# Optimization experiments

Measured on AMD Instinct MI355X. Metric: run time of the kernel, lower is better.

Reference implementation:

```python
import jax, jax.numpy as jnp
import numpy as np

N = 50000
E = 1600000
H, C = 4, 32
NEG_SLOPE = 0.2
EPS = 1e-16


def _l2norm_row(a):
    # F.normalize(a, p=2, dim=1) for a of shape [1, F]
    return a / jnp.maximum(jnp.linalg.norm(a, axis=1, keepdims=True), 1e-12)


def setup_inputs() -> dict:
    key = jax.random.key(0)
    ks = jax.random.split(key, 7)
    x = jax.random.normal(ks[0], (N, 256), dtype=jnp.float32)
    edge_index = jax.random.randint(ks[1], (2, E), 0, N, dtype=jnp.int32)
    v_mapping = jax.random.normal(ks[2], (64, 256), dtype=jnp.float32) * 0.1
    W_src = jax.random.normal(ks[3], (256, H * C), dtype=jnp.float32) * 0.06
    att_src = jax.random.normal(ks[4], (1, 64), dtype=jnp.float32)
    att_dst = jax.random.normal(ks[5], (1, 64), dtype=jnp.float32)
    bias = jnp.zeros((H * C,), dtype=jnp.float32)
    return {"x": x, "edge_index": edge_index, "v_mapping": v_mapping,
            "W_src": W_src, "att_src": att_src, "att_dst": att_dst, "bias": bias}


def reference(x, edge_index, v_mapping, W_src, att_src, att_dst, bias):
    # node projection: [N, H, C]
    x_proj = (x @ W_src).reshape(-1, H, C)
    # attention-locator scores: scalar per node
    score = x @ v_mapping.T                      # [N, F]
    a_src = (score * _l2norm_row(att_src)).sum(-1)  # [N]
    a_dst = (score * _l2norm_row(att_dst)).sum(-1)  # [N]

    src, dst = edge_index[0], edge_index[1]
    alpha = a_src[src] + a_dst[dst]              # [E]
    alpha = jax.nn.leaky_relu(alpha, NEG_SLOPE)
    # segment softmax over destination nodes
    m = jax.ops.segment_max(alpha, dst, num_segments=N)
    alpha = jnp.exp(alpha - jax.lax.stop_gradient(m)[dst])
    denom = jax.ops.segment_sum(alpha, dst, num_segments=N)
    alpha = alpha / (denom[dst] + EPS)           # [E]

    msg = x_proj[src] * alpha[:, None, None]     # [E, H, C]
    agg = jax.ops.segment_sum(msg, dst, num_segments=N)  # [N, H, C]

    out = x_proj + agg                           # residual as in forward
    out = out.reshape(-1, H * C) + bias          # concat heads + bias
    return out
```

## Files before the change

### kernel.cpp

```cpp
#include <hip/hip_runtime.h>

#define N_NODES 50000
#define E_EDGES 1600000
#define HC 128
#define NEG_SLOPE 0.2f
#define SM_EPS 1e-16f
#define NBKT 782
#define BKT_STRIDE 2600
#define EPB1 3072
#define NB1 521

typedef __attribute__((ext_vector_type(8))) short short8v;
typedef __attribute__((ext_vector_type(4))) float f32x4;

__device__ inline unsigned bf16pack(float a, float b) {
  unsigned ua = __float_as_uint(a), ub = __float_as_uint(b);
  ua = (ua + 0x7fffu + ((ua >> 16) & 1u)) >> 16;
  ub = (ub + 0x7fffu + ((ub >> 16) & 1u)) >> 16;
  return ua | (ub << 16);
}

__global__ __launch_bounds__(256) void k0_init(
    const float* __restrict__ v_mapping,
    const float* __restrict__ att_src,
    const float* __restrict__ att_dst,
    const float* __restrict__ W,
    unsigned short* __restrict__ wT,
    int* __restrict__ gcursor) {
  const int tid = threadIdx.x, bid = blockIdx.x;
  if (bid < 4) {
    const int i = bid * 256 + tid;
    if (i < NBKT) gcursor[i] = i * BKT_STRIDE;
  }

  __shared__ float wv[2][256];
  {
    const int j = tid;
    float ns = 0.f, nd = 0.f;
    for (int f = 0; f < 64; ++f) {
      float a = att_src[f]; ns = fmaf(a, a, ns);
      float b = att_dst[f]; nd = fmaf(b, b, nd);
    }
    ns = fmaxf(sqrtf(ns), 1e-12f);
    nd = fmaxf(sqrtf(nd), 1e-12f);
    float s = 0.f, d = 0.f;
    for (int f = 0; f < 64; ++f) {
      float v = v_mapping[f * 256 + j];
      s = fmaf(v, att_src[f], s);
      d = fmaf(v, att_dst[f], d);
    }
    wv[0][j] = s / ns;
    wv[1][j] = d / nd;
  }
  __syncthreads();

#pragma unroll
  for (int r = 0; r < 8; ++r) {
    const int n = bid * 8 + r;
    const int k = tid;
    float v;
    if (n < 128) v = W[k * 128 + n];
    else if (n == 128) v = wv[0][k];
    else if (n == 129) v = wv[1][k];
    else v = 0.f;
    unsigned u = __float_as_uint(v);
    u = (u + 0x7fffu + ((u >> 16) & 1u)) >> 16;
    wT[n * 256 + k] = (unsigned short)u;
  }
}

__global__ __launch_bounds__(256) void k1_node(
    const float* __restrict__ x,
    const unsigned short* __restrict__ wT,
    unsigned* __restrict__ xpb,
    float* __restrict__ a_src, float* __restrict__ a_dst) {
  __shared__ unsigned short xs[64 * 264];
  const int tid = threadIdx.x;
  const int w = tid >> 6, lane = tid & 63;
  const int rowbase = blockIdx.x * 64;

  const float4* x4 = (const float4*)x;
#pragma unroll
  for (int c = 0; c < 16; ++c) {
    const int idx = c * 256 + tid;
    const int row = idx >> 6, c4 = idx & 63;
    float4 v = make_float4(0.f, 0.f, 0.f, 0.f);
    if (rowbase + row < N_NODES) v = x4[(size_t)(rowbase + row) * 64 + c4];
    uint2 p;
    p.x = bf16pack(v.x, v.y);
    p.y = bf16pack(v.z, v.w);
    *(uint2*)&xs[row * 264 + c4 * 4] = p;
  }
  __syncthreads();

  f32x4 acc[9];
#pragma unroll
  for (int t = 0; t < 9; ++t) acc[t] = (f32x4){0.f, 0.f, 0.f, 0.f};

  const int m = lane & 15, kq = lane >> 4;
  const unsigned short* arow = &xs[(w * 16 + m) * 264 + kq * 8];
#pragma unroll
  for (int ks = 0; ks < 8; ++ks) {
    const short8v af = *(const short8v*)(arow + ks * 32);
#pragma unroll
    for (int ct = 0; ct < 9; ++ct) {
      const short8v bf = *(const short8v*)(wT + (ct * 16 + m) * 256 + ks * 32 + kq * 8);
      acc[ct] = __builtin_amdgcn_mfma_f32_16x16x32_bf16(af, bf, acc[ct], 0, 0, 0);
    }
  }

  if (m < 2) {
    float* ap = m ? a_dst : a_src;
#pragma unroll
    for (int i = 0; i < 4; ++i) {
      const int rg = rowbase + w * 16 + kq * 4 + i;
      if (rg < N_NODES) ap[rg] = acc[8][i];
    }
  }

  float* cs = (float*)&xs[w * 16 * 264];
#pragma unroll
  for (int ct = 0; ct < 8; ++ct)
#pragma unroll
    for (int i = 0; i < 4; ++i)
      cs[(kq * 4 + i) * 132 + ct * 16 + m] = acc[ct][i];
  __syncthreads();

  const int prow = lane & 15, q = lane >> 4;
  const int grow = rowbase + w * 16 + prow;
  unsigned uu[16];
#pragma unroll
  for (int u = 0; u < 16; ++u) {
    const float2 f2 = *(const float2*)&cs[prow * 132 + q * 32 + u * 2];
    uu[u] = bf16pack(f2.x, f2.y);
  }
  if (grow < N_NODES) {
    uint4* d4 = (uint4*)&xpb[(size_t)grow * 64 + q * 16];
    d4[0] = make_uint4(uu[0], uu[1], uu[2], uu[3]);
    d4[1] = make_uint4(uu[4], uu[5], uu[6], uu[7]);
    d4[2] = make_uint4(uu[8], uu[9], uu[10], uu[11]);
    d4[3] = make_uint4(uu[12], uu[13], uu[14], uu[15]);
  }
}

__global__ __launch_bounds__(1024) void kc1_coarse(
    const int* __restrict__ ei,
    const float* __restrict__ a_src, const float* __restrict__ a_dst,
    int* __restrict__ gcursor, int2* __restrict__ coarse) {
  __shared__ int chist[NBKT];
  __shared__ int gbase[NBKT];
  __shared__ int ccur[NBKT];
  const int tid = threadIdx.x;
  const int ebase = blockIdx.x * EPB1;
  for (int b = tid; b < NBKT; b += 1024) { chist[b] = 0; ccur[b] = 0; }
  __syncthreads();

#pragma unroll
  for (int i = 0; i < 3; ++i) {
    const int e = ebase + i * 1024 + tid;
    if (e < E_EDGES) atomicAdd(&chist[ei[E_EDGES + e] >> 6], 1);
  }
  __syncthreads();

  for (int b = tid; b < NBKT; b += 1024) {
    const int c = chist[b];
    if (c > 0) gbase[b] = atomicAdd(&gcursor[b], c);
  }
  __syncthreads();

#pragma unroll
  for (int i = 0; i < 3; ++i) {
    const int e = ebase + i * 1024 + tid;
    if (e < E_EDGES) {
      const int s = ei[e];
      const int d = ei[E_EDGES + e];
      const int b = d >> 6;
      float a = a_src[s] + a_dst[d];
      a = a > 0.f ? a : NEG_SLOPE * a;
      const float ev = __expf(a);
      const int pos = gbase[b] + atomicAdd(&ccur[b], 1);
      if (pos < (b + 1) * BKT_STRIDE)
        coarse[pos] = make_int2(s | ((d & 63) << 16), __float_as_int(ev));
    }
  }
}

__global__ __launch_bounds__(1024) void kc2_reduce(
    const int* __restrict__ gcursor, const int2* __restrict__ coarse,
    const unsigned* __restrict__ xpb,
    const float* __restrict__ bias,
    float* __restrict__ out) {
  __shared__ unsigned sorted[BKT_STRIDE];
  __shared__ int hist[64], cur[64];
  __shared__ int base[65];
  const int b = blockIdx.x;
  const int tid = threadIdx.x;
  const int cstart = b * BKT_STRIDE;
  const int cnt = min(gcursor[b] - cstart, BKT_STRIDE);

  if (tid < 64) { hist[tid] = 0; cur[tid] = 0; }
  __syncthreads();

  for (int j = tid; j < cnt; j += 1024)
    atomicAdd(&hist[(coarse[cstart + j].x >> 16) & 63], 1);
  __syncthreads();

  if (tid < 64) {
    const int h = hist[tid];
    int inc = h;
#pragma unroll
    for (int off = 1; off < 64; off <<= 1) {
      int t = __shfl_up(inc, off);
      if (tid >= off) inc += t;
    }
    base[tid] = inc - h;
    if (tid == 63) base[64] = inc;
  }
  __syncthreads();

  for (int j = tid; j < cnt; j += 1024) {
    const int2 e2 = coarse[cstart + j];
    const int dloc = (e2.x >> 16) & 63;
    unsigned uev = (unsigned)e2.y;
    uev = (uev + 0x7fffu + ((uev >> 16) & 1u)) >> 16;
    const int p = base[dloc] + atomicAdd(&cur[dloc], 1);
    sorted[p] = (unsigned)(e2.x & 0xffff) | (uev << 16);
  }
  __syncthreads();

  const int g = tid >> 4, gl = tid & 15;
  const int dst = (b << 6) | g;
  if (dst >= N_NODES) return;

  const uint4* xp4 = (const uint4*)xpb;
  const float4* br = (const float4*)bias;
  const float4 b0 = br[2 * gl], b1 = br[2 * gl + 1];

  const int s0 = base[g];
  const int cntd = base[g + 1] - s0;

  float acc[8];
#pragma unroll
  for (int i = 0; i < 8; ++i) acc[i] = 0.f;
  float den = 0.f;

  int j = 0;
  for (; j + 4 <= cntd; j += 4) {
    unsigned u[4];
    float ev[4];
    uint4 v[4];
#pragma unroll
    for (int t = 0; t < 4; ++t) {
      u[t] = sorted[s0 + j + t];
      ev[t] = __uint_as_float(u[t] & 0xffff0000u);
      v[t] = xp4[(size_t)(u[t] & 0xffffu) * 16 + gl];
    }
#pragma unroll
    for (int t = 0; t < 4; ++t) {
      den += ev[t];
      acc[0] = fmaf(ev[t], __uint_as_float(v[t].x << 16), acc[0]);
      acc[1] = fmaf(ev[t], __uint_as_float(v[t].x & 0xffff0000u), acc[1]);
      acc[2] = fmaf(ev[t], __uint_as_float(v[t].y << 16), acc[2]);
      acc[3] = fmaf(ev[t], __uint_as_float(v[t].y & 0xffff0000u), acc[3]);
      acc[4] = fmaf(ev[t], __uint_as_float(v[t].z << 16), acc[4]);
      acc[5] = fmaf(ev[t], __uint_as_float(v[t].z & 0xffff0000u), acc[5]);
      acc[6] = fmaf(ev[t], __uint_as_float(v[t].w << 16), acc[6]);
      acc[7] = fmaf(ev[t], __uint_as_float(v[t].w & 0xffff0000u), acc[7]);
    }
  }
  for (; j < cntd; ++j) {
    const unsigned u = sorted[s0 + j];
    const float ev = __uint_as_float(u & 0xffff0000u);
    const uint4 v = xp4[(size_t)(u & 0xffffu) * 16 + gl];
    den += ev;
    acc[0] = fmaf(ev, __uint_as_float(v.x << 16), acc[0]);
    acc[1] = fmaf(ev, __uint_as_float(v.x & 0xffff0000u), acc[1]);
    acc[2] = fmaf(ev, __uint_as_float(v.y << 16), acc[2]);
    acc[3] = fmaf(ev, __uint_as_float(v.y & 0xffff0000u), acc[3]);
    acc[4] = fmaf(ev, __uint_as_float(v.z << 16), acc[4]);
    acc[5] = fmaf(ev, __uint_as_float(v.z & 0xffff0000u), acc[5]);
    acc[6] = fmaf(ev, __uint_as_float(v.w << 16), acc[6]);
    acc[7] = fmaf(ev, __uint_as_float(v.w & 0xffff0000u), acc[7]);
  }

  const float inv = 1.f / (den + SM_EPS);
  const uint4 ur = xp4[(size_t)dst * 16 + gl];
  float4 o0, o1;
  o0.x = __uint_as_float(ur.x << 16)         + b0.x + acc[0] * inv;
  o0.y = __uint_as_float(ur.x & 0xffff0000u) + b0.y + acc[1] * inv;
  o0.z = __uint_as_float(ur.y << 16)         + b0.z + acc[2] * inv;
  o0.w = __uint_as_float(ur.y & 0xffff0000u) + b0.w + acc[3] * inv;
  o1.x = __uint_as_float(ur.z << 16)         + b1.x + acc[4] * inv;
  o1.y = __uint_as_float(ur.z & 0xffff0000u) + b1.y + acc[5] * inv;
  o1.z = __uint_as_float(ur.w << 16)         + b1.z + acc[6] * inv;
  o1.w = __uint_as_float(ur.w & 0xffff0000u) + b1.w + acc[7] * inv;
  float4* orow = (float4*)(out + (size_t)dst * HC);
  orow[2 * gl] = o0;
  orow[2 * gl + 1] = o1;
}

extern "C" void kernel_launch(void* const* d_in, const int* in_sizes, int n_in,
                              void* d_out, int out_size, void* d_ws, size_t ws_size,
                              hipStream_t stream) {
  const float* x         = (const float*)d_in[0];
  const int*   ei        = (const int*)d_in[1];
  const float* v_mapping = (const float*)d_in[2];
  const float* W_src     = (const float*)d_in[3];
  const float* att_src   = (const float*)d_in[4];
  const float* att_dst   = (const float*)d_in[5];
  const float* bias      = (const float*)d_in[6];
  float* out = (float*)d_out;

  char* ws = (char*)d_ws;
  unsigned*       xpb     = (unsigned*)ws;        ws += (size_t)N_NODES * 64 * 4;
  float*          a_src   = (float*)ws;           ws += (size_t)N_NODES * 4;
  float*          a_dst   = (float*)ws;           ws += (size_t)N_NODES * 4;
  unsigned short* wT      = (unsigned short*)ws;  ws += 144 * 256 * 2;
  int*            gcursor = (int*)ws;             ws += ((NBKT + 127) / 128) * 128 * 4;
  int2*           coarse  = (int2*)ws;            ws += (size_t)NBKT * BKT_STRIDE * 8;

  k0_init<<<18, 256, 0, stream>>>(v_mapping, att_src, att_dst, W_src, wT, gcursor);
  k1_node<<<(N_NODES + 63) / 64, 256, 0, stream>>>(x, wT, xpb, a_src, a_dst);
  kc1_coarse<<<NB1, 1024, 0, stream>>>(ei, a_src, a_dst, gcursor, coarse);
  kc2_reduce<<<NBKT, 1024, 0, stream>>>(gcursor, coarse, xpb, bias, out);
}
```

Baseline: 151.8 us.

## Fuse edge bucketing into node GEMM kernel and defer exp to reduce

```diff
diff --git a/kernel.cpp b/kernel.cpp
--- a/kernel.cpp
+++ b/kernel.cpp
@@ -7,8 +7,7 @@
 #define SM_EPS 1e-16f
 #define NBKT 782
 #define BKT_STRIDE 2600
-#define EPB1 3072
-#define NB1 521
+#define EPBH 2048
 
 typedef __attribute__((ext_vector_type(8))) short short8v;
 typedef __attribute__((ext_vector_type(4))) float f32x4;
@@ -69,15 +68,56 @@
   }
 }
 
-__global__ __launch_bounds__(256) void k1_node(
+__global__ __launch_bounds__(256) void k1_fused(
     const float* __restrict__ x,
     const unsigned short* __restrict__ wT,
     unsigned* __restrict__ xpb,
-    float* __restrict__ a_src, float* __restrict__ a_dst) {
-  __shared__ unsigned short xs[64 * 264];
+    float* __restrict__ a_src, float* __restrict__ a_dst,
+    const int* __restrict__ ei,
+    int* __restrict__ gcursor, unsigned* __restrict__ coarse) {
+  __shared__ char smem[64 * 264 * 2];
+  const int bid = blockIdx.x;
   const int tid = threadIdx.x;
+
+  if (bid & 1) {
+    int* chist = (int*)smem;
+    int* gbase = (int*)(smem + 3200);
+    int* ccur  = (int*)(smem + 6400);
+    const int ebase = (bid >> 1) * EPBH;
+    for (int b = tid; b < NBKT; b += 256) { chist[b] = 0; ccur[b] = 0; }
+    __syncthreads();
+
+#pragma unroll
+    for (int i = 0; i < 8; ++i) {
+      const int e = ebase + i * 256 + tid;
+      if (e < E_EDGES) atomicAdd(&chist[ei[E_EDGES + e] >> 6], 1);
+    }
+    __syncthreads();
+
+    for (int b = tid; b < NBKT; b += 256) {
+      const int c = chist[b];
+      if (c > 0) gbase[b] = atomicAdd(&gcursor[b], c);
+    }
+    __syncthreads();
+
+#pragma unroll
+    for (int i = 0; i < 8; ++i) {
+      const int e = ebase + i * 256 + tid;
+      if (e < E_EDGES) {
+        const int s = ei[e];
+        const int d = ei[E_EDGES + e];
+        const int b = d >> 6;
+        const int pos = gbase[b] + atomicAdd(&ccur[b], 1);
+        if (pos < (b + 1) * BKT_STRIDE)
+          coarse[pos] = (unsigned)s | ((unsigned)(d & 63) << 16);
+      }
+    }
+    return;
+  }
+
+  unsigned short* xs = (unsigned short*)smem;
   const int w = tid >> 6, lane = tid & 63;
-  const int rowbase = blockIdx.x * 64;
+  const int rowbase = (bid >> 1) * 64;
 
   const float4* x4 = (const float4*)x;
 #pragma unroll
@@ -118,7 +158,7 @@
     }
   }
 
-  float* cs = (float*)&xs[w * 16 * 264];
+  float* cs = (float*)(smem + (size_t)w * 16 * 264 * 2);
 #pragma unroll
   for (int ct = 0; ct < 8; ++ct)
 #pragma unroll
@@ -143,66 +183,30 @@
   }
 }
 
-__global__ __launch_bounds__(1024) void kc1_coarse(
-    const int* __restrict__ ei,
+__global__ __launch_bounds__(512) void kc2_reduce(
+    const int* __restrict__ gcursor, const unsigned* __restrict__ coarse,
     const float* __restrict__ a_src, const float* __restrict__ a_dst,
-    int* __restrict__ gcursor, int2* __restrict__ coarse) {
-  __shared__ int chist[NBKT];
-  __shared__ int gbase[NBKT];
-  __shared__ int ccur[NBKT];
-  const int tid = threadIdx.x;
-  const int ebase = blockIdx.x * EPB1;
-  for (int b = tid; b < NBKT; b += 1024) { chist[b] = 0; ccur[b] = 0; }
-  __syncthreads();
-
-#pragma unroll
-  for (int i = 0; i < 3; ++i) {
-    const int e = ebase + i * 1024 + tid;
-    if (e < E_EDGES) atomicAdd(&chist[ei[E_EDGES + e] >> 6], 1);
-  }
-  __syncthreads();
-
-  for (int b = tid; b < NBKT; b += 1024) {
-    const int c = chist[b];
-    if (c > 0) gbase[b] = atomicAdd(&gcursor[b], c);
-  }
-  __syncthreads();
-
-#pragma unroll
-  for (int i = 0; i < 3; ++i) {
-    const int e = ebase + i * 1024 + tid;
-    if (e < E_EDGES) {
-      const int s = ei[e];
-      const int d = ei[E_EDGES + e];
-      const int b = d >> 6;
-      float a = a_src[s] + a_dst[d];
-      a = a > 0.f ? a : NEG_SLOPE * a;
-      const float ev = __expf(a);
-      const int pos = gbase[b] + atomicAdd(&ccur[b], 1);
-      if (pos < (b + 1) * BKT_STRIDE)
-        coarse[pos] = make_int2(s | ((d & 63) << 16), __float_as_int(ev));
-    }
-  }
-}
-
-__global__ __launch_bounds__(1024) void kc2_reduce(
-    const int* __restrict__ gcursor, const int2* __restrict__ coarse,
     const unsigned* __restrict__ xpb,
     const float* __restrict__ bias,
     float* __restrict__ out) {
   __shared__ unsigned sorted[BKT_STRIDE];
   __shared__ int hist[64], cur[64];
   __shared__ int base[65];
+  __shared__ float adl[64];
   const int b = blockIdx.x;
   const int tid = threadIdx.x;
   const int cstart = b * BKT_STRIDE;
   const int cnt = min(gcursor[b] - cstart, BKT_STRIDE);
 
-  if (tid < 64) { hist[tid] = 0; cur[tid] = 0; }
-  __syncthreads();
-
-  for (int j = tid; j < cnt; j += 1024)
-    atomicAdd(&hist[(coarse[cstart + j].x >> 16) & 63], 1);
+  if (tid < 64) {
+    hist[tid] = 0; cur[tid] = 0;
+    const int dg = (b << 6) | tid;
+    adl[tid] = (dg < N_NODES) ? a_dst[dg] : 0.f;
+  }
+  __syncthreads();
+
+  for (int j = tid; j < cnt; j += 512)
+    atomicAdd(&hist[(coarse[cstart + j] >> 16) & 63], 1);
   __syncthreads();
 
   if (tid < 64) {
@@ -218,85 +222,89 @@
   }
   __syncthreads();
 
-  for (int j = tid; j < cnt; j += 1024) {
-    const int2 e2 = coarse[cstart + j];
-    const int dloc = (e2.x >> 16) & 63;
-    unsigned uev = (unsigned)e2.y;
+  for (int j = tid; j < cnt; j += 512) {
+    const unsigned e2 = coarse[cstart + j];
+    const int src = e2 & 0xffffu;
+    const int dloc = (e2 >> 16) & 63;
+    float a = a_src[src] + adl[dloc];
+    a = a > 0.f ? a : NEG_SLOPE * a;
+    unsigned uev = __float_as_uint(__expf(a));
     uev = (uev + 0x7fffu + ((uev >> 16) & 1u)) >> 16;
     const int p = base[dloc] + atomicAdd(&cur[dloc], 1);
-    sorted[p] = (unsigned)(e2.x & 0xffff) | (uev << 16);
+    sorted[p] = (unsigned)src | (uev << 16);
   }
   __syncthreads();
 
   const int g = tid >> 4, gl = tid & 15;
-  const int dst = (b << 6) | g;
-  if (dst >= N_NODES) return;
-
   const uint4* xp4 = (const uint4*)xpb;
   const float4* br = (const float4*)bias;
   const float4 b0 = br[2 * gl], b1 = br[2 * gl + 1];
 
-  const int s0 = base[g];
-  const int cntd = base[g + 1] - s0;
-
-  float acc[8];
-#pragma unroll
-  for (int i = 0; i < 8; ++i) acc[i] = 0.f;
-  float den = 0.f;
-
-  int j = 0;
-  for (; j + 4 <= cntd; j += 4) {
-    unsigned u[4];
-    float ev[4];
-    uint4 v[4];
-#pragma unroll
-    for (int t = 0; t < 4; ++t) {
-      u[t] = sorted[s0 + j + t];
-      ev[t] = __uint_as_float(u[t] & 0xffff0000u);
-      v[t] = xp4[(size_t)(u[t] & 0xffffu) * 16 + gl];
-    }
-#pragma unroll
-    for (int t = 0; t < 4; ++t) {
-      den += ev[t];
-      acc[0] = fmaf(ev[t], __uint_as_float(v[t].x << 16), acc[0]);
-      acc[1] = fmaf(ev[t], __uint_as_float(v[t].x & 0xffff0000u), acc[1]);
-      acc[2] = fmaf(ev[t], __uint_as_float(v[t].y << 16), acc[2]);
-      acc[3] = fmaf(ev[t], __uint_as_float(v[t].y & 0xffff0000u), acc[3]);
-      acc[4] = fmaf(ev[t], __uint_as_float(v[t].z << 16), acc[4]);
-      acc[5] = fmaf(ev[t], __uint_as_float(v[t].z & 0xffff0000u), acc[5]);
-      acc[6] = fmaf(ev[t], __uint_as_float(v[t].w << 16), acc[6]);
-      acc[7] = fmaf(ev[t], __uint_as_float(v[t].w & 0xffff0000u), acc[7]);
-    }
-  }
-  for (; j < cntd; ++j) {
-    const unsigned u = sorted[s0 + j];
-    const float ev = __uint_as_float(u & 0xffff0000u);
-    const uint4 v = xp4[(size_t)(u & 0xffffu) * 16 + gl];
-    den += ev;
-    acc[0] = fmaf(ev, __uint_as_float(v.x << 16), acc[0]);
-    acc[1] = fmaf(ev, __uint_as_float(v.x & 0xffff0000u), acc[1]);
-    acc[2] = fmaf(ev, __uint_as_float(v.y << 16), acc[2]);
-    acc[3] = fmaf(ev, __uint_as_float(v.y & 0xffff0000u), acc[3]);
-    acc[4] = fmaf(ev, __uint_as_float(v.z << 16), acc[4]);
-    acc[5] = fmaf(ev, __uint_as_float(v.z & 0xffff0000u), acc[5]);
-    acc[6] = fmaf(ev, __uint_as_float(v.w << 16), acc[6]);
-    acc[7] = fmaf(ev, __uint_as_float(v.w & 0xffff0000u), acc[7]);
-  }
-
-  const float inv = 1.f / (den + SM_EPS);
-  const uint4 ur = xp4[(size_t)dst * 16 + gl];
-  float4 o0, o1;
-  o0.x = __uint_as_float(ur.x << 16)         + b0.x + acc[0] * inv;
-  o0.y = __uint_as_float(ur.x & 0xffff0000u) + b0.y + acc[1] * inv;
-  o0.z = __uint_as_float(ur.y << 16)         + b0.z + acc[2] * inv;
-  o0.w = __uint_as_float(ur.y & 0xffff0000u) + b0.w + acc[3] * inv;
-  o1.x = __uint_as_float(ur.z << 16)         + b1.x + acc[4] * inv;
-  o1.y = __uint_as_float(ur.z & 0xffff0000u) + b1.y + acc[5] * inv;
-  o1.z = __uint_as_float(ur.w << 16)         + b1.z + acc[6] * inv;
-  o1.w = __uint_as_float(ur.w & 0xffff0000u) + b1.w + acc[7] * inv;
-  float4* orow = (float4*)(out + (size_t)dst * HC);
-  orow[2 * gl] = o0;
-  orow[2 * gl + 1] = o1;
+  for (int dl = g; dl < 64; dl += 32) {
+    const int dst = (b << 6) | dl;
+    if (dst >= N_NODES) break;
+    const int s0 = base[dl];
+    const int cntd = base[dl + 1] - s0;
+
+    float acc[8];
+#pragma unroll
+    for (int i = 0; i < 8; ++i) acc[i] = 0.f;
+    float den = 0.f;
+
+    int j = 0;
+    for (; j + 4 <= cntd; j += 4) {
+      unsigned u[4];
+      float ev[4];
+      uint4 v[4];
+#pragma unroll
+      for (int t = 0; t < 4; ++t) {
+        u[t] = sorted[s0 + j + t];
+        ev[t] = __uint_as_float(u[t] & 0xffff0000u);
+        v[t] = xp4[(size_t)(u[t] & 0xffffu) * 16 + gl];
+      }
+#pragma unroll
+      for (int t = 0; t < 4; ++t) {
+        den += ev[t];
+        acc[0] = fmaf(ev[t], __uint_as_float(v[t].x << 16), acc[0]);
+        acc[1] = fmaf(ev[t], __uint_as_float(v[t].x & 0xffff0000u), acc[1]);
+        acc[2] = fmaf(ev[t], __uint_as_float(v[t].y << 16), acc[2]);
+        acc[3] = fmaf(ev[t], __uint_as_float(v[t].y & 0xffff0000u), acc[3]);
+        acc[4] = fmaf(ev[t], __uint_as_float(v[t].z << 16), acc[4]);
+        acc[5] = fmaf(ev[t], __uint_as_float(v[t].z & 0xffff0000u), acc[5]);
+        acc[6] = fmaf(ev[t], __uint_as_float(v[t].w << 16), acc[6]);
+        acc[7] = fmaf(ev[t], __uint_as_float(v[t].w & 0xffff0000u), acc[7]);
+      }
+    }
+    for (; j < cntd; ++j) {
+      const unsigned u = sorted[s0 + j];
+      const float ev = __uint_as_float(u & 0xffff0000u);
+      const uint4 v = xp4[(size_t)(u & 0xffffu) * 16 + gl];
+      den += ev;
+      acc[0] = fmaf(ev, __uint_as_float(v.x << 16), acc[0]);
+      acc[1] = fmaf(ev, __uint_as_float(v.x & 0xffff0000u), acc[1]);
+      acc[2] = fmaf(ev, __uint_as_float(v.y << 16), acc[2]);
+      acc[3] = fmaf(ev, __uint_as_float(v.y & 0xffff0000u), acc[3]);
+      acc[4] = fmaf(ev, __uint_as_float(v.z << 16), acc[4]);
+      acc[5] = fmaf(ev, __uint_as_float(v.z & 0xffff0000u), acc[5]);
+      acc[6] = fmaf(ev, __uint_as_float(v.w << 16), acc[6]);
+      acc[7] = fmaf(ev, __uint_as_float(v.w & 0xffff0000u), acc[7]);
+    }
+
+    const float inv = 1.f / (den + SM_EPS);
+    const uint4 ur = xp4[(size_t)dst * 16 + gl];
+    float4 o0, o1;
+    o0.x = __uint_as_float(ur.x << 16)         + b0.x + acc[0] * inv;
+    o0.y = __uint_as_float(ur.x & 0xffff0000u) + b0.y + acc[1] * inv;
+    o0.z = __uint_as_float(ur.y << 16)         + b0.z + acc[2] * inv;
+    o0.w = __uint_as_float(ur.y & 0xffff0000u) + b0.w + acc[3] * inv;
+    o1.x = __uint_as_float(ur.z << 16)         + b1.x + acc[4] * inv;
+    o1.y = __uint_as_float(ur.z & 0xffff0000u) + b1.y + acc[5] * inv;
+    o1.z = __uint_as_float(ur.w << 16)         + b1.z + acc[6] * inv;
+    o1.w = __uint_as_float(ur.w & 0xffff0000u) + b1.w + acc[7] * inv;
+    float4* orow = (float4*)(out + (size_t)dst * HC);
+    orow[2 * gl] = o0;
+    orow[2 * gl + 1] = o1;
+  }
 }
 
 extern "C" void kernel_launch(void* const* d_in, const int* in_sizes, int n_in,
@@ -317,10 +325,9 @@
   float*          a_dst   = (float*)ws;           ws += (size_t)N_NODES * 4;
   unsigned short* wT      = (unsigned short*)ws;  ws += 144 * 256 * 2;
   int*            gcursor = (int*)ws;             ws += ((NBKT + 127) / 128) * 128 * 4;
-  int2*           coarse  = (int2*)ws;            ws += (size_t)NBKT * BKT_STRIDE * 8;
+  unsigned*       coarse  = (unsigned*)ws;        ws += (size_t)NBKT * BKT_STRIDE * 4;
 
   k0_init<<<18, 256, 0, stream>>>(v_mapping, att_src, att_dst, W_src, wT, gcursor);
-  k1_node<<<(N_NODES + 63) / 64, 256, 0, stream>>>(x, wT, xpb, a_src, a_dst);
-  kc1_coarse<<<NB1, 1024, 0, stream>>>(ei, a_src, a_dst, gcursor, coarse);
-  kc2_reduce<<<NBKT, 1024, 0, stream>>>(gcursor, coarse, xpb, bias, out);
-}
+  k1_fused<<<2 * NBKT, 256, 0, stream>>>(x, wT, xpb, a_src, a_dst, ei, gcursor, coarse);
+  kc2_reduce<<<NBKT, 512, 0, stream>>>(gcursor, coarse, a_src, a_dst, xpb, bias, out);
+}
```

Result: no change. 148.8 us (-1.9%).
